# Kernel tuning notes

Hardware: AMD Instinct MI355X
Metric: run time of the kernel (lower is better)

Reference implementation:

```python
import jax, jax.numpy as jnp
import numpy as np

L, T, B, H = 2, 512, 64, 1024


def setup_inputs() -> dict:
    key = jax.random.key(0)
    ks = jax.random.split(key, 6)
    std = 1.0 / np.sqrt(H)
    uni = lambda k, shp: jax.random.uniform(k, shp, jnp.float32, -std, std)
    return {
        "x": jax.random.normal(ks[0], (T, B, H), jnp.float32),
        "h0": jnp.zeros((L, B, H), jnp.float32),
        "c0": jnp.zeros((L, B, H), jnp.float32),
        "i2h_w": uni(ks[1], (L, 4 * H, H)),
        "i2h_b": uni(ks[2], (L, 4 * H)),
        "h2h_w": uni(ks[3], (L, 4 * H, H)),
        "h2h_b": uni(ks[4], (L, 4 * H)),
    }


def _layer(x_seq, h, c, Wi, bi, Wh, bh):
    # Precompute input projection for all timesteps: [T, B, 4H]
    xp = jnp.einsum('tbi,gi->tbg', x_seq, Wi) + bi

    def step(carry, xp_t):
        h, c = carry
        preact = xp_t + h @ Wh.T + bh          # [B, 4H]
        ig, fg, gg, og = jnp.split(preact, 4, axis=-1)
        ig = jax.nn.sigmoid(ig)
        fg = jax.nn.sigmoid(fg)
        gg = jnp.tanh(gg)
        og = jax.nn.sigmoid(og)
        c = c * fg + ig * gg
        h = og * jnp.tanh(c)
        return (h, c), (h, c)

    _, (hs, cs) = jax.lax.scan(step, (h, c), xp)
    return hs, cs  # each [T, B, H]


def reference(x, h0, c0, i2h_w, i2h_b, h2h_w, h2h_b):
    output_hs, output_cs = [], []
    hs = x
    for l in range(L):
        hs, cs = _layer(hs, h0[l], c0[l], i2h_w[l], i2h_b[l], h2h_w[l], h2h_b[l])
        # dropout=0 so dropout layer is identity
        output_hs.append(hs[-1])
        # NOTE: original code has a bug: appends hs[-1] for cs too; replicated.
        output_cs.append(hs[-1])
    output_hs = jnp.stack(output_hs, axis=0)  # [L, B, H]
    output_cs = jnp.stack(output_cs, axis=0)
    return (hs, (output_hs, output_cs))
```

## Files before the change

kernel.cpp:

```cpp
#include <hip/hip_runtime.h>
#include <hip/hip_bf16.h>
#include <math.h>


#define Hh 1024
#define Bb 64
#define Tt 512
#define BH (Bb*Hh)
#define G4 (4*Hh)

typedef __bf16 v8bf __attribute__((ext_vector_type(8)));
typedef float  v4f  __attribute__((ext_vector_type(4)));
typedef int    v4i  __attribute__((ext_vector_type(4)));
typedef unsigned long long u64;
typedef __hip_bfloat16 bf16;

__device__ __forceinline__ bf16 f2bf(float v){ return __float2bfloat16(v); }

__device__ __forceinline__ v8bf cvt8(const float* p) {
    v4f a = *(const v4f*)p;
    v4f b = *(const v4f*)(p + 4);
    v8bf r;
    #pragma unroll
    for (int i = 0; i < 4; ++i) {
        r[i]   = __builtin_bit_cast(__bf16, f2bf(a[i]));
        r[i+4] = __builtin_bit_cast(__bf16, f2bf(b[i]));
    }
    return r;
}

__device__ __forceinline__ v8bf ld8bf_agent(const bf16* p) {
    const u64* q = (const u64*)p;
    u64 a = __hip_atomic_load(q,     __ATOMIC_RELAXED, __HIP_MEMORY_SCOPE_AGENT);
    u64 b = __hip_atomic_load(q + 1, __ATOMIC_RELAXED, __HIP_MEMORY_SCOPE_AGENT);
    union { u64 v[2]; v8bf r; } u;
    u.v[0] = a; u.v[1] = b;
    return u.r;
}

__device__ __forceinline__ float fast_sigmoid(float x) {
    x = fminf(fmaxf(x, -30.f), 30.f);
    return 1.f / (1.f + __expf(-x));
}
__device__ __forceinline__ float fast_tanh(float x) {
    x = fminf(fmaxf(x, -15.f), 15.f);
    float e = __expf(2.f * x);
    return (e - 1.f) / (e + 1.f);
}

__global__ void init_ws(const float* __restrict__ h0,
                        bf16* __restrict__ hout, unsigned int* __restrict__ bar) {
    int i = blockIdx.x * blockDim.x + threadIdx.x;
    if (i == 0) *bar = 0u;
    hout[(0*2 + 1)*BH + i] = f2bf(h0[i]);
    hout[(1*2 + 0)*BH + i] = f2bf(h0[BH + i]);
}

__global__ __launch_bounds__(1024, 4)
void lstm_persist(const float* __restrict__ x,
                  const float* __restrict__ wi, const float* __restrict__ bi,
                  const float* __restrict__ wh, const float* __restrict__ bh,
                  const float* __restrict__ c0,
                  bf16* __restrict__ hout,
                  float* __restrict__ out, unsigned int* __restrict__ bar)
{
    const int layer  = blockIdx.x >> 7;
    const int jslice = blockIdx.x & 127;
    const int jbase  = jslice * 8;

    const int tid  = threadIdx.x;
    const int lane = tid & 63;
    const int w    = tid >> 6;
    const int ks   = w >> 3;
    const int kh   = (w >> 2) & 1;
    const int rt   = w & 3;
    const int s    = w >> 2;
    const int quad = lane >> 4;
    const int l15  = lane & 15;

    const float* W = (ks ? wh : wi) + (size_t)layer * G4 * Hh;
    v8bf Breg[16][2];
    #pragma unroll
    for (int ct = 0; ct < 2; ++ct) {
        const int n    = ct*16 + l15;
        const int grow = (n >> 3)*Hh + jbase + (n & 7);
        const float* wp = W + (size_t)grow * Hh + kh*512 + quad*8;
        #pragma unroll
        for (int kk = 0; kk < 16; ++kk)
            Breg[kk][ct] = cvt8(wp + kk*32);
    }

    const int arow = rt*16 + l15;
    const size_t aoff = (size_t)arow * Hh + kh*512 + quad*8;

    const int eb  = tid >> 2;
    const int ejp = tid & 3;
    float bsum[4][2];
    float c_reg[2] = {0.f, 0.f};
    if (tid < 256) {
        #pragma unroll
        for (int gi = 0; gi < 4; ++gi) {
            #pragma unroll
            for (int u = 0; u < 2; ++u) {
                int bo = layer*G4 + gi*Hh + jbase + 2*ejp + u;
                bsum[gi][u] = bi[bo] + bh[bo];
            }
        }
        #pragma unroll
        for (int u = 0; u < 2; ++u)
            c_reg[u] = c0[(size_t)layer*BH + eb*Hh + jbase + 2*ejp + u];
    }

    __shared__ float part[4][64][36];

    for (int p = 0; p <= Tt; ++p) {
        const int t = p - layer;
        const bool act = (t >= 0) & (t < Tt);

        if (act) {
            v4f acc0 = {0.f,0.f,0.f,0.f}, acc1 = {0.f,0.f,0.f,0.f};
            if (ks == 0 && layer == 0) {
                const float* ap = x + (size_t)t*BH + aoff;
                #pragma unroll
                for (int kk = 0; kk < 16; ++kk) {
                    v8bf af = cvt8(ap + kk*32);
                    acc0 = __builtin_amdgcn_mfma_f32_16x16x32_bf16(af, Breg[kk][0], acc0, 0,0,0);
                    acc1 = __builtin_amdgcn_mfma_f32_16x16x32_bf16(af, Breg[kk][1], acc1, 0,0,0);
                }
            } else {
                const int srcbuf = (ks == 0) ? ((p-1) & 1)
                                             : (layer*2 + ((p-1) & 1));
                const bf16* ap = hout + (size_t)srcbuf*BH + aoff;
                #pragma unroll
                for (int kk = 0; kk < 16; ++kk) {
                    v8bf af = ld8bf_agent(ap + kk*32);
                    acc0 = __builtin_amdgcn_mfma_f32_16x16x32_bf16(af, Breg[kk][0], acc0, 0,0,0);
                    acc1 = __builtin_amdgcn_mfma_f32_16x16x32_bf16(af, Breg[kk][1], acc1, 0,0,0);
                }
            }
            #pragma unroll
            for (int r = 0; r < 4; ++r) {
                part[s][rt*16 + quad*4 + r][l15]      = acc0[r];
                part[s][rt*16 + quad*4 + r][16 + l15] = acc1[r];
            }
        }
        __syncthreads();

        if (tid < 256 && act) {
            float g[4][2];
            #pragma unroll
            for (int gi = 0; gi < 4; ++gi) {
                int c = gi*8 + 2*ejp;
                g[gi][0] = part[0][eb][c]   + part[1][eb][c]
                         + part[2][eb][c]   + part[3][eb][c]   + bsum[gi][0];
                g[gi][1] = part[0][eb][c+1] + part[1][eb][c+1]
                         + part[2][eb][c+1] + part[3][eb][c+1] + bsum[gi][1];
            }
            float hv[2];
            #pragma unroll
            for (int u = 0; u < 2; ++u) {
                float ig = fast_sigmoid(g[0][u]);
                float fg = fast_sigmoid(g[1][u]);
                float gv = fast_tanh(g[2][u]);
                float og = fast_sigmoid(g[3][u]);
                c_reg[u] = c_reg[u]*fg + ig*gv;
                hv[u] = og * fast_tanh(c_reg[u]);
            }

            const int idx = eb*Hh + jbase + 2*ejp;
            unsigned int hp =
                  (unsigned int)__builtin_bit_cast(unsigned short, f2bf(hv[0]))
                | ((unsigned int)__builtin_bit_cast(unsigned short, f2bf(hv[1])) << 16);
            __hip_atomic_store((unsigned int*)(hout + (size_t)(layer*2 + (p & 1))*BH + idx),
                               hp, __ATOMIC_RELAXED, __HIP_MEMORY_SCOPE_AGENT);
            if (layer == 1) {
                float2 o; o.x = hv[0]; o.y = hv[1];
                *(float2*)(out + (size_t)t*BH + idx) = o;
            }
            if (t == Tt-1) {
                float2 o; o.x = hv[0]; o.y = hv[1];
                *(float2*)(out + (size_t)Tt*BH + (size_t)layer*BH + idx)       = o;
                *(float2*)(out + (size_t)Tt*BH + (size_t)(2 + layer)*BH + idx) = o;
            }
        }

        if (p < Tt) {
            __syncthreads();
            if (tid == 0) {
                __hip_atomic_fetch_add(bar, 1u, __ATOMIC_RELAXED, __HIP_MEMORY_SCOPE_AGENT);
                const unsigned int target = (unsigned int)(p + 1) * 256u;
                while (__hip_atomic_load(bar, __ATOMIC_RELAXED, __HIP_MEMORY_SCOPE_AGENT) < target)
                    __builtin_amdgcn_s_sleep(2);
            }
            __syncthreads();
        }
    }
}

extern "C" void kernel_launch(void* const* d_in, const int* in_sizes, int n_in,
                              void* d_out, int out_size, void* d_ws, size_t ws_size,
                              hipStream_t stream) {
    const float* x  = (const float*)d_in[0];
    const float* h0 = (const float*)d_in[1];
    const float* c0 = (const float*)d_in[2];
    const float* wi = (const float*)d_in[3];
    const float* bi = (const float*)d_in[4];
    const float* wh = (const float*)d_in[5];
    const float* bh = (const float*)d_in[6];
    float* out = (float*)d_out;

    char* ws = (char*)d_ws;
    unsigned int* bar = (unsigned int*)ws;
    bf16* hout = (bf16*)(ws + 256);

    init_ws<<<256, 256, 0, stream>>>(h0, hout, bar);
    lstm_persist<<<256, 1024, 0, stream>>>(x, wi, bi, wh, bh, c0,
                                           hout, out, bar);
}
```

Measured before the change: 14.39 ms.

## Shard grid barrier counters and software-pipeline recurrent h loads with inline asm

Replaces the single global barrier counter with 16 counters on separate 64-byte lines. Each block increments one of them, and a whole wavefront polls all 16 in parallel, which spreads atomic contention across cache lines. The recurrent h loads become inline-asm global_load_dwordx4 with sc0 sc1 (cache-bypassing), issued in groups of four with explicit vmcnt waits, so loads overlap the MFMAs instead of running as serialized atomic 64-bit loads. This relies on hand-counted waitcnts and sched_barriers, and the workspace layout shifts to make room for the counters.

```diff
diff --git a/kernel.cpp b/kernel.cpp
--- a/kernel.cpp
+++ b/kernel.cpp
@@ -11,7 +11,6 @@
 
 typedef __bf16 v8bf __attribute__((ext_vector_type(8)));
 typedef float  v4f  __attribute__((ext_vector_type(4)));
-typedef int    v4i  __attribute__((ext_vector_type(4)));
 typedef unsigned long long u64;
 typedef __hip_bfloat16 bf16;
 
@@ -29,15 +28,6 @@
     return r;
 }
 
-__device__ __forceinline__ v8bf ld8bf_agent(const bf16* p) {
-    const u64* q = (const u64*)p;
-    u64 a = __hip_atomic_load(q,     __ATOMIC_RELAXED, __HIP_MEMORY_SCOPE_AGENT);
-    u64 b = __hip_atomic_load(q + 1, __ATOMIC_RELAXED, __HIP_MEMORY_SCOPE_AGENT);
-    union { u64 v[2]; v8bf r; } u;
-    u.v[0] = a; u.v[1] = b;
-    return u.r;
-}
-
 __device__ __forceinline__ float fast_sigmoid(float x) {
     x = fminf(fmaxf(x, -30.f), 30.f);
     return 1.f / (1.f + __expf(-x));
@@ -48,10 +38,29 @@
     return (e - 1.f) / (e + 1.f);
 }
 
+#define ISS4(buf, base) do {                                                   \
+    asm volatile("global_load_dwordx4 %0, %1, off sc0 sc1"                     \
+                 : "=v"(buf[0]) : "v"(ap + (base+0)*32));                      \
+    asm volatile("global_load_dwordx4 %0, %1, off sc0 sc1"                     \
+                 : "=v"(buf[1]) : "v"(ap + (base+1)*32));                      \
+    asm volatile("global_load_dwordx4 %0, %1, off sc0 sc1"                     \
+                 : "=v"(buf[2]) : "v"(ap + (base+2)*32));                      \
+    asm volatile("global_load_dwordx4 %0, %1, off sc0 sc1"                     \
+                 : "=v"(buf[3]) : "v"(ap + (base+3)*32));                      \
+} while (0)
+
+#define MFMA4(buf, base) do {                                                  \
+    _Pragma("unroll")                                                          \
+    for (int k = 0; k < 4; ++k) {                                              \
+        acc0 = __builtin_amdgcn_mfma_f32_16x16x32_bf16(buf[k], Breg[(base)+k][0], acc0, 0,0,0); \
+        acc1 = __builtin_amdgcn_mfma_f32_16x16x32_bf16(buf[k], Breg[(base)+k][1], acc1, 0,0,0); \
+    }                                                                          \
+} while (0)
+
 __global__ void init_ws(const float* __restrict__ h0,
                         bf16* __restrict__ hout, unsigned int* __restrict__ bar) {
     int i = blockIdx.x * blockDim.x + threadIdx.x;
-    if (i == 0) *bar = 0u;
+    if (i < 256) bar[i] = 0u;
     hout[(0*2 + 1)*BH + i] = f2bf(h0[i]);
     hout[(1*2 + 0)*BH + i] = f2bf(h0[BH + i]);
 }
@@ -131,12 +140,26 @@
                 const int srcbuf = (ks == 0) ? ((p-1) & 1)
                                              : (layer*2 + ((p-1) & 1));
                 const bf16* ap = hout + (size_t)srcbuf*BH + aoff;
-                #pragma unroll
-                for (int kk = 0; kk < 16; ++kk) {
-                    v8bf af = ld8bf_agent(ap + kk*32);
-                    acc0 = __builtin_amdgcn_mfma_f32_16x16x32_bf16(af, Breg[kk][0], acc0, 0,0,0);
-                    acc1 = __builtin_amdgcn_mfma_f32_16x16x32_bf16(af, Breg[kk][1], acc1, 0,0,0);
-                }
+                v8bf afA[4], afB[4];
+                ISS4(afA, 0);
+                ISS4(afB, 4);
+                asm volatile("s_waitcnt vmcnt(4)");
+                __builtin_amdgcn_sched_barrier(0);
+                MFMA4(afA, 0);
+                __builtin_amdgcn_sched_barrier(0);
+                ISS4(afA, 8);
+                asm volatile("s_waitcnt vmcnt(4)");
+                __builtin_amdgcn_sched_barrier(0);
+                MFMA4(afB, 4);
+                __builtin_amdgcn_sched_barrier(0);
+                ISS4(afB, 12);
+                asm volatile("s_waitcnt vmcnt(4)");
+                __builtin_amdgcn_sched_barrier(0);
+                MFMA4(afA, 8);
+                __builtin_amdgcn_sched_barrier(0);
+                asm volatile("s_waitcnt vmcnt(0)");
+                __builtin_amdgcn_sched_barrier(0);
+                MFMA4(afB, 12);
             }
             #pragma unroll
             for (int r = 0; r < 4; ++r) {
@@ -186,11 +209,19 @@
 
         if (p < Tt) {
             __syncthreads();
-            if (tid == 0) {
-                __hip_atomic_fetch_add(bar, 1u, __ATOMIC_RELAXED, __HIP_MEMORY_SCOPE_AGENT);
-                const unsigned int target = (unsigned int)(p + 1) * 256u;
-                while (__hip_atomic_load(bar, __ATOMIC_RELAXED, __HIP_MEMORY_SCOPE_AGENT) < target)
-                    __builtin_amdgcn_s_sleep(2);
+            if (w == 0) {
+                if (lane == 0)
+                    __hip_atomic_fetch_add(bar + (blockIdx.x & 15)*16, 1u,
+                                           __ATOMIC_RELAXED, __HIP_MEMORY_SCOPE_AGENT);
+                const unsigned int tgt = (unsigned int)(p + 1) * 16u;
+                bool done = (lane >= 16);
+                while (!__all(done)) {
+                    if (!done)
+                        done = (__hip_atomic_load(bar + lane*16, __ATOMIC_RELAXED,
+                                                  __HIP_MEMORY_SCOPE_AGENT) >= tgt);
+                    if (!__all(done))
+                        __builtin_amdgcn_s_sleep(2);
+                }
             }
             __syncthreads();
         }
@@ -211,7 +242,7 @@
 
     char* ws = (char*)d_ws;
     unsigned int* bar = (unsigned int*)ws;
-    bf16* hout = (bf16*)(ws + 256);
+    bf16* hout = (bf16*)(ws + 1024);
 
     init_ws<<<256, 256, 0, stream>>>(h0, hout, bar);
     lstm_persist<<<256, 1024, 0, stream>>>(x, wi, bi, wh, bh, c0,
```

Result: faster. 12.50 ms (-13.2%).
